# Performance work log

Hardware: AMD Instinct MI355X
Metric: run time of the kernel (lower is better)

Reference implementation:

```python
import jax, jax.numpy as jnp
import numpy as np

# Model dims
D = 64          # node channels (dim)
M = 16          # msg_channels
DEPTH = 3
VOCAB = 21      # num_atom_tokens
N = 100000      # nodes
E = 1600000     # directed edges
EIN = 2 * D + 1            # edge_mlp input: [x_i, x_j, |rel|^2]
EH = 2 * EIN               # dim_expansion * edge_input_dim
CH = 4 * M                 # 2 * dim_expansion * msg_channels
NH = 2 * D                 # dim_expansion * in_channels
INIT_STD = 1e-3            # init_eps normal init for Linear weights


def setup_inputs() -> dict:
    key = jax.random.key(0)
    ks = jax.random.split(key, 16)
    feats = jax.random.randint(ks[0], (N,), 0, VOCAB, dtype=jnp.int32)
    coors = jax.random.normal(ks[1], (N, 3), dtype=jnp.float32) * 10.0
    edge_index = jax.random.randint(ks[2], (2, E), 0, N, dtype=jnp.int32)
    emb = jax.random.normal(ks[3], (VOCAB, D), dtype=jnp.float32) * 0.1
    f32 = jnp.float32
    return {
        "feats": feats, "coors": coors, "edge_index": edge_index, "emb": emb,
        # edge_mlp: Linear(EIN->EH), SiLU, Linear(EH->M), SiLU
        "We1": jax.random.normal(ks[4], (DEPTH, EIN, EH), f32) * INIT_STD,
        "be1": jnp.zeros((DEPTH, EH), f32),
        "We2": jax.random.normal(ks[5], (DEPTH, EH, M), f32) * INIT_STD,
        "be2": jnp.zeros((DEPTH, M), f32),
        # coord_mlp: Linear(M->CH), SiLU, Linear(CH->1)
        "Wc1": jax.random.normal(ks[6], (DEPTH, M, CH), f32) * INIT_STD,
        "bc1": jnp.zeros((DEPTH, CH), f32),
        "Wc2": jax.random.normal(ks[7], (DEPTH, CH, 1), f32) * INIT_STD,
        "bc2": jnp.zeros((DEPTH, 1), f32),
        # node_mlp: Linear(D+M->NH), SiLU, Linear(NH->D)
        "Wn1": jax.random.normal(ks[8], (DEPTH, D + M, NH), f32) * INIT_STD,
        "bn1": jnp.zeros((DEPTH, NH), f32),
        "Wn2": jax.random.normal(ks[9], (DEPTH, NH, D), f32) * INIT_STD,
        "bn2": jnp.zeros((DEPTH, D), f32),
    }


def reference(feats, coors, edge_index, emb,
              We1, be1, We2, be2, Wc1, bc1, Wc2, bc2, Wn1, bn1, Wn2, bn2):
    # node_encoder: embedding lookup
    x = emb[feats]                       # [N, D]
    pos = coors                          # [N, 3]
    src = edge_index[0]                  # x_j / pos_j (source, flow source->target)
    tgt = edge_index[1]                  # x_i / pos_i (target) = scatter index
    n = x.shape[0]
    for l in range(DEPTH):
        # message: per-edge gather + MLPs
        rel = pos[tgt] - pos[src]                              # [E, 3]
        d2 = jnp.sum(rel * rel, axis=1, keepdims=True)         # [E, 1]
        m_in = jnp.concatenate([x[tgt], x[src], d2], axis=1)   # [E, 2D+1]
        h = jax.nn.silu(m_in @ We1[l] + be1[l])                # [E, EH]
        msg = jax.nn.silu(h @ We2[l] + be2[l])                 # [E, M]
        cw = jax.nn.silu(msg @ Wc1[l] + bc1[l]) @ Wc2[l] + bc2[l]  # [E, 1]
        pos_msg = rel * cw                                     # [E, 3] (coors_norm is Identity)
        # aggregate: scatter-add to target nodes
        agg_msg = jax.ops.segment_sum(msg, tgt, num_segments=n)      # [N, M]
        agg_pos = jax.ops.segment_sum(pos_msg, tgt, num_segments=n)  # [N, 3]
        # node update: node_norm is Identity
        nh = jax.nn.silu(jnp.concatenate([x, agg_msg], axis=1) @ Wn1[l] + bn1[l])
        out_x = nh @ Wn2[l] + bn2[l]                           # [N, D]
        pos = pos + agg_pos                                    # out_pos += pos (no velocity)
        x = x + out_x                                          # residual=True
    return x, pos
```

## Files before the change

kernel.cpp:

```cpp
#include <hip/hip_runtime.h>
#include <hip/hip_bf16.h>
#include <stdint.h>

#define NDIM   64
#define MDIM   16
#define NLAYER 3
#define EIN    129
#define EHD    258
#define CHD    64
#define NHD    128
#define NIN    80
#define AB_STRIDE 512
#define PKT_STRIDE 32
#define FP8_SCALE 1024.0f
#define NVALS  19

#define WE1F_L (34*2*512)
#define WN1F_L (8*3*512)
#define WN2F_L (4*4*512)
#define WE2F_L (9*512)
#define WC1F_L (4*512)

typedef float vf2 __attribute__((ext_vector_type(2)));
typedef __bf16 bf16x8 __attribute__((ext_vector_type(8)));
typedef float  f32x4  __attribute__((ext_vector_type(4)));

#define MFMA16(a, b, c) __builtin_amdgcn_mfma_f32_16x16x32_bf16((a), (b), (c), 0, 0, 0)

__device__ __forceinline__ float rcp_f(float x) { return __builtin_amdgcn_rcpf(x); }
#if __has_builtin(__builtin_amdgcn_exp2f)
__device__ __forceinline__ float exp2_f(float x) { return __builtin_amdgcn_exp2f(x); }
#else
__device__ __forceinline__ float exp2_f(float x) { return __expf(x * 0.6931471805599453f); }
#endif
__device__ __forceinline__ float silu_f(float v) {
    return v * rcp_f(1.0f + __expf(-v));
}
#define CC_EXP (-1.4426950408889634f / 1024.0f)
__device__ __forceinline__ float hprime_f(float u) {
    return u * rcp_f(1.0f + exp2_f(CC_EXP * u));
}
__device__ __forceinline__ float bflo(uint32_t u) {
    union { uint32_t u; float f; } c; c.u = u << 16; return c.f;
}
__device__ __forceinline__ float bfhi(uint32_t u) {
    union { uint32_t u; float f; } c; c.u = u & 0xffff0000u; return c.f;
}
__device__ __forceinline__ uint32_t pk_fp8_4(float f0, float f1, float f2, float f3) {
    uint32_t r = (uint32_t)__builtin_amdgcn_cvt_pk_fp8_f32(f0, f1, 0, false);
    r = (uint32_t)__builtin_amdgcn_cvt_pk_fp8_f32(f2, f3, (int)r, true);
    return r;
}
__device__ __forceinline__ float clamp8(float v) {
    return fminf(448.0f, fmaxf(-448.0f, v * FP8_SCALE));
}

__global__ void prep_kernel(const float* __restrict__ We1, const float* __restrict__ Wn1,
                            const float* __restrict__ Wn2, const float* __restrict__ We2,
                            const float* __restrict__ Wc1,
                            __bf16* __restrict__ WE1F, __bf16* __restrict__ WN1F,
                            __bf16* __restrict__ WN2F, __bf16* __restrict__ WE2F,
                            __bf16* __restrict__ WC1F) {
    int idx = blockIdx.x * 256 + threadIdx.x;
    const int T1 = NLAYER * WE1F_L;
    if (idx < T1) {
        int l  = idx / WE1F_L;
        int r  = idx % WE1F_L;
        int ct = r / 1024;
        int r2 = r % 1024;
        int kh = r2 / 512;
        int r3 = r2 % 512;
        int lane = r3 >> 3, jj = r3 & 7;
        int half = ct / 17, ctl = ct % 17;
        int col = ctl * 16 + (lane & 15);
        int k = kh * 32 + (lane >> 4) * 8 + jj;
        float v = 0.f;
        if (col < EHD) v = We1[((size_t)l * EIN + (half ? 64 + k : k)) * EHD + col];
        WE1F[idx] = (__bf16)v;
        return;
    }
    idx -= T1;
    const int T2 = NLAYER * WN1F_L;
    if (idx < T2) {
        int l  = idx / WN1F_L;
        int r  = idx % WN1F_L;
        int ct = r / 1536;
        int r2 = r % 1536;
        int kt = r2 / 512;
        int r3 = r2 % 512;
        int lane = r3 >> 3, jj = r3 & 7;
        int col = ct * 16 + (lane & 15);
        int k = kt * 32 + (lane >> 4) * 8 + jj;
        float v = (k < NIN) ? Wn1[((size_t)l * NIN + k) * NHD + col] : 0.f;
        WN1F[idx] = (__bf16)v;
        return;
    }
    idx -= T2;
    const int T3 = NLAYER * WN2F_L;
    if (idx < T3) {
        int l  = idx / WN2F_L;
        int r  = idx % WN2F_L;
        int ct = r / 2048;
        int r2 = r % 2048;
        int kt = r2 / 512;
        int r3 = r2 % 512;
        int lane = r3 >> 3, jj = r3 & 7;
        int col = ct * 16 + (lane & 15);
        int k = kt * 32 + (lane >> 4) * 8 + jj;
        WN2F[idx] = (__bf16)Wn2[((size_t)l * NHD + k) * NDIM + col];
        return;
    }
    idx -= T3;
    const int T4 = NLAYER * WE2F_L;
    if (idx < T4) {
        int l  = idx / WE2F_L;
        int r  = idx % WE2F_L;
        int kt = r / 512;
        int r3 = r % 512;
        int lane = r3 >> 3, jj = r3 & 7;
        int m = lane & 15;
        int k = kt * 32 + (lane >> 4) * 8 + jj;
        float v = (k < EHD) ? We2[((size_t)l * EHD + k) * MDIM + m] * (1.0f / FP8_SCALE) : 0.f;
        WE2F[idx] = (__bf16)v;
        return;
    }
    idx -= T4;
    const int T5 = NLAYER * WC1F_L;
    if (idx < T5) {
        int l  = idx / WC1F_L;
        int r  = idx % WC1F_L;
        int ct = r / 512;
        int r3 = r % 512;
        int lane = r3 >> 3, jj = r3 & 7;
        int c = ct * 16 + (lane & 15);
        int k = (lane >> 4) * 8 + jj;
        float v = (k < MDIM) ? Wc1[((size_t)l * MDIM + k) * CHD + c] : 0.f;
        WC1F[idx] = (__bf16)v;
    }
}

__global__ void init_kernel(const int* __restrict__ feats, const float* __restrict__ coors,
                            const float* __restrict__ emb,
                            float* __restrict__ x, float* __restrict__ pos, int N) {
    int idx = blockIdx.x * 256 + threadIdx.x;
    int nx = N * NDIM;
    if (idx < nx) {
        int n = idx >> 6, c = idx & 63;
        x[idx] = emb[feats[n] * NDIM + c];
    } else {
        int j = idx - nx;
        if (j < N * 3) pos[j] = coors[j];
    }
}

__global__ void hist_kernel(const int* __restrict__ ei, int* __restrict__ cnt, int E) {
    int e = blockIdx.x * 256 + threadIdx.x;
    if (e < E) atomicAdd(&cnt[ei[E + e]], 1);
}

__global__ void scan_sum_kernel(const int* __restrict__ cnt, int* __restrict__ bsum, int N) {
    __shared__ int ws[4];
    int i = blockIdx.x * 256 + threadIdx.x;
    int v = (i < N) ? cnt[i] : 0;
    #pragma unroll
    for (int off = 32; off; off >>= 1) v += __shfl_down(v, off);
    int lane = threadIdx.x & 63, w = threadIdx.x >> 6;
    if (lane == 0) ws[w] = v;
    __syncthreads();
    if (threadIdx.x == 0) bsum[blockIdx.x] = ws[0] + ws[1] + ws[2] + ws[3];
}
__global__ void __launch_bounds__(1024) scan_top_kernel(int* __restrict__ bsum, int nb) {
    __shared__ int ws[16];
    int tid = threadIdx.x, lane = tid & 63, w = tid >> 6;
    int v = (tid < nb) ? bsum[tid] : 0;
    int sc = v;
    #pragma unroll
    for (int off = 1; off < 64; off <<= 1) {
        int u = __shfl_up(sc, off);
        if (lane >= off) sc += u;
    }
    if (lane == 63) ws[w] = sc;
    __syncthreads();
    int woff = 0;
    #pragma unroll
    for (int k = 0; k < 16; ++k) woff += (k < w) ? ws[k] : 0;
    if (tid < nb) bsum[tid] = woff + sc - v;
}
__global__ void scan_fin_kernel(const int* __restrict__ cnt, const int* __restrict__ bsum,
                                int* __restrict__ cursor, int N) {
    __shared__ int ws[4];
    int i = blockIdx.x * 256 + threadIdx.x;
    int tid = threadIdx.x, lane = tid & 63, w = tid >> 6;
    int v = (i < N) ? cnt[i] : 0;
    int sc = v;
    #pragma unroll
    for (int off = 1; off < 64; off <<= 1) {
        int u = __shfl_up(sc, off);
        if (lane >= off) sc += u;
    }
    if (lane == 63) ws[w] = sc;
    __syncthreads();
    int woff = 0;
    #pragma unroll
    for (int k = 0; k < 4; ++k) woff += (k < w) ? ws[k] : 0;
    if (i < N) cursor[i] = bsum[blockIdx.x] + woff + sc - v;
}

__global__ void scatter_kernel(const int* __restrict__ ei, int* __restrict__ cursor,
                               uint2* __restrict__ sorted_st, int E) {
    int e = blockIdx.x * 256 + threadIdx.x;
    if (e >= E) return;
    int s = ei[e], t = ei[E + e];
    int p = atomicAdd(&cursor[t], 1);
    uint2 st; st.x = (uint32_t)s; st.y = (uint32_t)t;
    sorted_st[p] = st;
}

__global__ void __launch_bounds__(256) gemm_ab_mfma(
        const float* __restrict__ x, const float* __restrict__ pos,
        const bf16x8* __restrict__ WE1Fl, const float* __restrict__ be1l,
        uint8_t* __restrict__ A8, uint8_t* __restrict__ pkt,
        float* __restrict__ agg_msg, float* __restrict__ agg_pos, int N) {
    __shared__ __align__(16) __bf16 stg[4][16][280];
    int wave = threadIdx.x >> 6, lane = threadIdx.x & 63;
    int half = wave & 1;
    int nb = blockIdx.x * 32 + (wave >> 1) * 16;
    int lrow = lane & 15, lkg = lane >> 4;
    int row = nb + lrow; if (row >= N) row = N - 1;

    const float* xr = x + (size_t)row * NDIM + lkg * 8;
    bf16x8 a0, a1;
    #pragma unroll
    for (int j = 0; j < 8; ++j) { a0[j] = (__bf16)xr[j]; a1[j] = (__bf16)xr[32 + j]; }

    f32x4 acc[17];
    #pragma unroll
    for (int t = 0; t < 17; ++t) acc[t] = (f32x4){0.f, 0.f, 0.f, 0.f};
    const bf16x8* bf = WE1Fl + (size_t)(half * 17) * 2 * 64 + lane;
    #pragma unroll
    for (int t = 0; t < 17; ++t) {
        bf16x8 b0 = bf[(t * 2 + 0) * 64];
        bf16x8 b1 = bf[(t * 2 + 1) * 64];
        acc[t] = MFMA16(a0, b0, acc[t]);
        acc[t] = MFMA16(a1, b1, acc[t]);
    }
    #pragma unroll
    for (int t = 0; t < 17; ++t) {
        int col = t * 16 + lrow;
        float bias = (half == 0 && col < EHD) ? be1l[col] : 0.f;
        #pragma unroll
        for (int r = 0; r < 4; ++r)
            stg[wave][lkg * 4 + r][col] = (__bf16)(acc[t][r] + bias);
    }
    __syncthreads();

    int node = lane >> 2;
    int gnode = nb + node;
    const __bf16* hrow = &stg[wave][node][(lane & 3) * 64];
    if (gnode < N) {
        uint8_t* dst = A8 + (size_t)gnode * AB_STRIDE + half * 256 + (lane & 3) * 64;
        #pragma unroll
        for (int g = 0; g < 8; ++g) {
            bf16x8 hv = *(const bf16x8*)(hrow + g * 8);
            uint2 pk;
            pk.x = pk_fp8_4(clamp8((float)hv[0]), clamp8((float)hv[1]),
                            clamp8((float)hv[2]), clamp8((float)hv[3]));
            pk.y = pk_fp8_4(clamp8((float)hv[4]), clamp8((float)hv[5]),
                            clamp8((float)hv[6]), clamp8((float)hv[7]));
            *(uint2*)(dst + g * 8) = pk;
        }
    }
    if (lane < 16 && nb + lane < N) {
        int gn = nb + lane;
        const uint16_t* hr = (const uint16_t*)&stg[wave][lane][256];
        uint32_t ex = (uint32_t)hr[0] | ((uint32_t)hr[1] << 16);
        uint32_t* pk = (uint32_t*)(pkt + (size_t)gn * PKT_STRIDE);
        if (half == 0) {
            uint4 w0;
            w0.x = __float_as_uint(pos[3 * gn]);
            w0.y = __float_as_uint(pos[3 * gn + 1]);
            w0.z = __float_as_uint(pos[3 * gn + 2]);
            w0.w = ex;
            *(uint4*)pk = w0;
        } else {
            pk[4] = ex;
        }
    }
    {
        int i16 = blockIdx.x * 512 + (int)threadIdx.x * 2;
        if (i16 + 1 < N * MDIM) {
            *(vf2*)(agg_msg + i16) = (vf2){0.f, 0.f};
        } else if (i16 < N * MDIM) {
            agg_msg[i16] = 0.f;
        }
        if (threadIdx.x < 96) {
            int ip = blockIdx.x * 96 + (int)threadIdx.x;
            if (ip < N * 3) agg_pos[ip] = 0.f;
        }
    }
}

__global__ void __launch_bounds__(256) edge_kernel(
        const uint2* __restrict__ sorted_st,
        const uint8_t* __restrict__ A8, const uint8_t* __restrict__ pkt,
        const bf16x8* __restrict__ WE2Fl, const bf16x8* __restrict__ WC1Fl,
        const float* __restrict__ be2l,
        const float* __restrict__ bc1, const float* __restrict__ Wc2,
        const float* __restrict__ bc2, const float* __restrict__ w128,
        float* __restrict__ agg_msg, float* __restrict__ agg_pos, int E) {

    __shared__ __align__(16) vf2    w128p[132];
    __shared__ __align__(16) __bf16 msg_lds[4][64][24];
    __shared__ int  run_t[4][64];
    __shared__ uint run_se[4][64];

    int tid  = threadIdx.x;
    int wave = tid >> 6, lane = tid & 63;
    int kg   = lane >> 4, lrow = lane & 15;

    int base = blockIdx.x * 256 + wave * 64;
    int eo = base + lane;
    bool active = (eo < E);
    int eoc = active ? eo : (E - 1);
    uint2 st = sorted_st[eoc];
    int s_own = (int)st.x;
    int t_ld  = (int)st.y;
    int t_scan = active ? t_ld : -1;

    const uint32_t* ppt = (const uint32_t*)(pkt + (size_t)t_ld  * PKT_STRIDE);
    const uint32_t* pps = (const uint32_t*)(pkt + (size_t)s_own * PKT_STRIDE);
    uint4 pt0 = *(const uint4*)ppt;
    uint4 ps0 = *(const uint4*)pps;
    uint32_t b2o = pps[4];
    uint32_t a2o = pt0.w;
    float rx = __uint_as_float(pt0.x) - __uint_as_float(ps0.x);
    float ry = __uint_as_float(pt0.y) - __uint_as_float(ps0.y);
    float rz = __uint_as_float(pt0.z) - __uint_as_float(ps0.z);
    float d2o = rx*rx + ry*ry + rz*rz;

    bf16x8 bw[9];
    #pragma unroll
    for (int kt = 0; kt < 9; ++kt) bw[kt] = WE2Fl[kt * 64 + lane];
    bf16x8 bwc[4];
    float bc1r[4], wc2r[4];
    #pragma unroll
    for (int ct = 0; ct < 4; ++ct) {
        bwc[ct]  = WC1Fl[ct * 64 + lane];
        bc1r[ct] = bc1[ct * 16 + lrow];
        wc2r[ct] = Wc2[ct * 16 + lrow];
    }
    float be2m = be2l[lrow];
    float cb2  = bc2[0];

    for (int i = tid; i < 132; i += 256) {
        int k0 = i * 2;
        float lo = (k0     < EHD) ? w128[k0]     * FP8_SCALE : 0.f;
        float hi = (k0 + 1 < EHD) ? w128[k0 + 1] * FP8_SCALE : 0.f;
        w128p[i] = (vf2){lo, hi};
    }
    __syncthreads();

    #pragma unroll
    for (int tt = 0; tt < 4; ++tt) {
        int srcl = tt * 16 + lrow;
        int t_r = __shfl(t_ld, srcl);
        int s_r = __shfl(s_own, srcl);
        float d2r = __shfl(d2o, srcl);
        uint32_t a2r = (uint32_t)__shfl((int)a2o, srcl);
        uint32_t b2r = (uint32_t)__shfl((int)b2o, srcl);
        vf2 d2v = (vf2){d2r, d2r};

        const uint8_t* Ar = A8 + (size_t)t_r * AB_STRIDE + kg * 8;
        const uint8_t* Br = A8 + (size_t)s_r * AB_STRIDE + 256 + kg * 8;

        f32x4 acc = (f32x4){0.f, 0.f, 0.f, 0.f};
        #pragma unroll
        for (int kt = 0; kt < 8; ++kt) {
            uint2 ad = *(const uint2*)(Ar + kt * 32);
            uint2 bd = *(const uint2*)(Br + kt * 32);
            const vf2* wp = &w128p[kt * 16 + kg * 4];
            vf2 u0 = __builtin_amdgcn_cvt_pk_f32_fp8(ad.x, false)
                   + __builtin_amdgcn_cvt_pk_f32_fp8(bd.x, false) + d2v * wp[0];
            vf2 u1 = __builtin_amdgcn_cvt_pk_f32_fp8(ad.x, true)
                   + __builtin_amdgcn_cvt_pk_f32_fp8(bd.x, true)  + d2v * wp[1];
            vf2 u2 = __builtin_amdgcn_cvt_pk_f32_fp8(ad.y, false)
                   + __builtin_amdgcn_cvt_pk_f32_fp8(bd.y, false) + d2v * wp[2];
            vf2 u3 = __builtin_amdgcn_cvt_pk_f32_fp8(ad.y, true)
                   + __builtin_amdgcn_cvt_pk_f32_fp8(bd.y, true)  + d2v * wp[3];
            bf16x8 af;
            af[0] = (__bf16)hprime_f(u0.x); af[1] = (__bf16)hprime_f(u0.y);
            af[2] = (__bf16)hprime_f(u1.x); af[3] = (__bf16)hprime_f(u1.y);
            af[4] = (__bf16)hprime_f(u2.x); af[5] = (__bf16)hprime_f(u2.y);
            af[6] = (__bf16)hprime_f(u3.x); af[7] = (__bf16)hprime_f(u3.y);
            acc = MFMA16(af, bw[kt], acc);
        }
        {
            float h0 = 0.f, h1 = 0.f;
            if (kg == 0) {
                vf2 wx = w128p[128];
                float u0 = (bflo(a2r) + bflo(b2r)) * FP8_SCALE + d2r * wx.x;
                float u1 = (bfhi(a2r) + bfhi(b2r)) * FP8_SCALE + d2r * wx.y;
                h0 = hprime_f(u0);
                h1 = hprime_f(u1);
            }
            bf16x8 af;
            af[0] = (__bf16)h0; af[1] = (__bf16)h1;
            #pragma unroll
            for (int j = 2; j < 8; ++j) af[j] = (__bf16)0.f;
            acc = MFMA16(af, bw[8], acc);
        }
        #pragma unroll
        for (int r = 0; r < 4; ++r) {
            float mval = silu_f(acc[r] + be2m);
            msg_lds[wave][tt * 16 + kg * 4 + r][lrow] = (__bf16)mval;
        }
        __builtin_amdgcn_wave_barrier();

        bf16x8 ac = (bf16x8){(__bf16)0.f,(__bf16)0.f,(__bf16)0.f,(__bf16)0.f,
                             (__bf16)0.f,(__bf16)0.f,(__bf16)0.f,(__bf16)0.f};
        if (kg < 2) ac = *(const bf16x8*)&msg_lds[wave][tt * 16 + lrow][kg * 8];
        f32x4 c0 = (f32x4){0.f,0.f,0.f,0.f}, c1 = c0, c2 = c0, c3 = c0;
        c0 = MFMA16(ac, bwc[0], c0);
        c1 = MFMA16(ac, bwc[1], c1);
        c2 = MFMA16(ac, bwc[2], c2);
        c3 = MFMA16(ac, bwc[3], c3);
        float p0 = 0.f, p1 = 0.f, p2 = 0.f, p3 = 0.f;
        p0 += silu_f(c0[0] + bc1r[0]) * wc2r[0]; p1 += silu_f(c0[1] + bc1r[0]) * wc2r[0];
        p2 += silu_f(c0[2] + bc1r[0]) * wc2r[0]; p3 += silu_f(c0[3] + bc1r[0]) * wc2r[0];
        p0 += silu_f(c1[0] + bc1r[1]) * wc2r[1]; p1 += silu_f(c1[1] + bc1r[1]) * wc2r[1];
        p2 += silu_f(c1[2] + bc1r[1]) * wc2r[1]; p3 += silu_f(c1[3] + bc1r[1]) * wc2r[1];
        p0 += silu_f(c2[0] + bc1r[2]) * wc2r[2]; p1 += silu_f(c2[1] + bc1r[2]) * wc2r[2];
        p2 += silu_f(c2[2] + bc1r[2]) * wc2r[2]; p3 += silu_f(c2[3] + bc1r[2]) * wc2r[2];
        p0 += silu_f(c3[0] + bc1r[3]) * wc2r[3]; p1 += silu_f(c3[1] + bc1r[3]) * wc2r[3];
        p2 += silu_f(c3[2] + bc1r[3]) * wc2r[3]; p3 += silu_f(c3[3] + bc1r[3]) * wc2r[3];
        #pragma unroll
        for (int mk = 1; mk < 16; mk <<= 1) {
            p0 += __shfl_xor(p0, mk);
            p1 += __shfl_xor(p1, mk);
            p2 += __shfl_xor(p2, mk);
            p3 += __shfl_xor(p3, mk);
        }
        if (lrow < 4) {
            float sel = (lrow == 0) ? p0 : (lrow == 1) ? p1 : (lrow == 2) ? p2 : p3;
            msg_lds[wave][tt * 16 + kg * 4 + lrow][16] = (__bf16)(cb2 + sel);
        }
        __builtin_amdgcn_wave_barrier();
    }

    float cwo = (float)msg_lds[wave][lane][16];
    msg_lds[wave][lane][16] = (__bf16)(rx * cwo);
    msg_lds[wave][lane][17] = (__bf16)(ry * cwo);
    msg_lds[wave][lane][18] = (__bf16)(rz * cwo);

    int t_next = __shfl_down(t_scan, 1);
    bool is_end = (lane == 63) || (t_next != t_scan);
    uint64_t mask = __ballot(is_end);
    int nr = __popcll(mask);
    if (is_end) {
        uint64_t below = mask & ((1ULL << lane) - 1ULL);
        int rid = __popcll(below);
        int st2 = (below == 0ULL) ? 0 : (64 - __builtin_clzll(below));
        run_t[wave][rid]  = t_scan;
        run_se[wave][rid] = (uint)((st2 << 8) | lane);
    }
    __builtin_amdgcn_wave_barrier();

    for (int task = lane; task < nr * NVALS; task += 64) {
        int rid = task / NVALS;
        int v   = task - rid * NVALS;
        int t   = run_t[wave][rid];
        if (t >= 0) {
            uint se = run_se[wave][rid];
            int st2 = (int)(se >> 8), en = (int)(se & 0xFFu);
            float sum = 0.f;
            for (int e = st2; e <= en; ++e) sum += (float)msg_lds[wave][e][v];
            if (v < 16) atomicAdd(&agg_msg[(size_t)t * MDIM + v], sum);
            else        atomicAdd(&agg_pos[(size_t)t * 3 + (v - 16)], sum);
        }
    }
}

__global__ void __launch_bounds__(256) node_mfma(
        float* __restrict__ x, float* __restrict__ pos,
        const float* __restrict__ agg_msg, const float* __restrict__ agg_pos,
        const bf16x8* __restrict__ WN1Fl, const bf16x8* __restrict__ WN2Fl,
        const float* __restrict__ bn1l, const float* __restrict__ bn2l, int N) {
    __shared__ __align__(16) __bf16 stg[4][16][136];
    int wave = threadIdx.x >> 6, lane = threadIdx.x & 63;
    int nb = blockIdx.x * 64 + wave * 16;
    int lrow = lane & 15, lkg = lane >> 4;
    int row = nb + lrow;
    int rc = (row < N) ? row : (N - 1);

    const float* xr = x + (size_t)rc * NDIM + lkg * 8;
    bf16x8 a0, a1, a2;
    #pragma unroll
    for (int j = 0; j < 8; ++j) { a0[j] = (__bf16)xr[j]; a1[j] = (__bf16)xr[32 + j]; }
    if (lkg < 2) {
        const float* mr = agg_msg + (size_t)rc * MDIM + lkg * 8;
        #pragma unroll
        for (int j = 0; j < 8; ++j) a2[j] = (__bf16)mr[j];
    } else {
        #pragma unroll
        for (int j = 0; j < 8; ++j) a2[j] = (__bf16)0.f;
    }

    f32x4 h[8];
    #pragma unroll
    for (int t = 0; t < 8; ++t) h[t] = (f32x4){0.f, 0.f, 0.f, 0.f};
    const bf16x8* b1 = WN1Fl + lane;
    #pragma unroll
    for (int t = 0; t < 8; ++t) {
        h[t] = MFMA16(a0, b1[(t * 3 + 0) * 64], h[t]);
        h[t] = MFMA16(a1, b1[(t * 3 + 1) * 64], h[t]);
        h[t] = MFMA16(a2, b1[(t * 3 + 2) * 64], h[t]);
    }
    #pragma unroll
    for (int t = 0; t < 8; ++t) {
        int col = t * 16 + lrow;
        float bias = bn1l[col];
        #pragma unroll
        for (int r = 0; r < 4; ++r)
            stg[wave][lkg * 4 + r][col] = (__bf16)silu_f(h[t][r] + bias);
    }
    __syncthreads();

    bf16x8 af[4];
    #pragma unroll
    for (int kt = 0; kt < 4; ++kt)
        af[kt] = *(const bf16x8*)&stg[wave][lrow][kt * 32 + lkg * 8];

    f32x4 o[4];
    #pragma unroll
    for (int t = 0; t < 4; ++t) o[t] = (f32x4){0.f, 0.f, 0.f, 0.f};
    const bf16x8* b2 = WN2Fl + lane;
    #pragma unroll
    for (int t = 0; t < 4; ++t) {
        #pragma unroll
        for (int kt = 0; kt < 4; ++kt)
            o[t] = MFMA16(af[kt], b2[(t * 4 + kt) * 64], o[t]);
    }

    int orow = nb + lkg * 4;
    #pragma unroll
    for (int t = 0; t < 4; ++t) {
        int col = t * 16 + lrow;
        float bias = bn2l[col];
        #pragma unroll
        for (int r = 0; r < 4; ++r) {
            int rr = orow + r;
            if (rr < N) x[(size_t)rr * NDIM + col] += o[t][r] + bias;
        }
    }
    if (threadIdx.x < 192) {
        long j = (long)blockIdx.x * 192 + threadIdx.x;
        if (j < (long)N * 3) pos[j] += agg_pos[j];
    }
}

extern "C" void kernel_launch(void* const* d_in, const int* in_sizes, int n_in,
                              void* d_out, int out_size, void* d_ws, size_t ws_size,
                              hipStream_t stream) {
    const int*   feats = (const int*)  d_in[0];
    const float* coors = (const float*)d_in[1];
    const int*   ei    = (const int*)  d_in[2];
    const float* emb   = (const float*)d_in[3];
    const float* We1   = (const float*)d_in[4];
    const float* be1   = (const float*)d_in[5];
    const float* We2   = (const float*)d_in[6];
    const float* be2   = (const float*)d_in[7];
    const float* Wc1   = (const float*)d_in[8];
    const float* bc1   = (const float*)d_in[9];
    const float* Wc2   = (const float*)d_in[10];
    const float* bc2   = (const float*)d_in[11];
    const float* Wn1   = (const float*)d_in[12];
    const float* bn1   = (const float*)d_in[13];
    const float* Wn2   = (const float*)d_in[14];
    const float* bn2   = (const float*)d_in[15];

    const int N = in_sizes[0];
    const int E = in_sizes[2] / 2;

    float* x   = (float*)d_out;
    float* pos = (float*)d_out + (size_t)N * NDIM;

    char* w = (char*)d_ws;
    uint8_t* A8 = (uint8_t*)w;
    size_t off = ((size_t)N * AB_STRIDE + 255) & ~(size_t)255;
    uint8_t* pkt = (uint8_t*)(w + off);
    off += ((size_t)N * PKT_STRIDE + 255) & ~(size_t)255;
    float* agg_msg = (float*)(w + off);
    off += ((size_t)N * MDIM * 4 + 255) & ~(size_t)255;
    float* agg_pos = (float*)(w + off);
    off += ((size_t)N * 3 * 4 + 255) & ~(size_t)255;
    uint2* sorted_st = (uint2*)(w + off);
    off += ((size_t)E * 8 + 255) & ~(size_t)255;
    int* cnt = (int*)(w + off);
    off += ((size_t)N * 4 + 255) & ~(size_t)255;
    int* cursor = (int*)(w + off);
    off += ((size_t)N * 4 + 255) & ~(size_t)255;
    int* bsum = (int*)(w + off);
    off += (((size_t)N / 256 + 2) * 4 + 255) & ~(size_t)255;
    __bf16* WE1F = (__bf16*)(w + off);
    off += ((size_t)NLAYER * WE1F_L * 2 + 255) & ~(size_t)255;
    __bf16* WN1F = (__bf16*)(w + off);
    off += ((size_t)NLAYER * WN1F_L * 2 + 255) & ~(size_t)255;
    __bf16* WN2F = (__bf16*)(w + off);
    off += ((size_t)NLAYER * WN2F_L * 2 + 255) & ~(size_t)255;
    __bf16* WE2F = (__bf16*)(w + off);
    off += ((size_t)NLAYER * WE2F_L * 2 + 255) & ~(size_t)255;
    __bf16* WC1F = (__bf16*)(w + off);
    (void)ws_size; (void)n_in; (void)out_size;

    {
        int total = NLAYER * (WE1F_L + WN1F_L + WN2F_L + WE2F_L + WC1F_L);
        prep_kernel<<<(total + 255) / 256, 256, 0, stream>>>(We1, Wn1, Wn2, We2, Wc1,
                                                             WE1F, WN1F, WN2F, WE2F, WC1F);
    }
    {
        int total = N * (NDIM + 3);
        init_kernel<<<(total + 255) / 256, 256, 0, stream>>>(feats, coors, emb, x, pos, N);
    }
    hipMemsetAsync(cnt, 0, (size_t)N * 4, stream);
    hist_kernel<<<(E + 255) / 256, 256, 0, stream>>>(ei, cnt, E);
    {
        int nb = (N + 255) / 256;
        scan_sum_kernel<<<nb, 256, 0, stream>>>(cnt, bsum, N);
        scan_top_kernel<<<1, 1024, 0, stream>>>(bsum, nb);
        scan_fin_kernel<<<nb, 256, 0, stream>>>(cnt, bsum, cursor, N);
    }
    scatter_kernel<<<(E + 255) / 256, 256, 0, stream>>>(ei, cursor, sorted_st, E);

    for (int l = 0; l < NLAYER; ++l) {
        const float* We1_l  = We1 + (size_t)l * EIN * EHD;
        const float* w128_l = We1_l + (size_t)128 * EHD;

        gemm_ab_mfma<<<(N + 31) / 32, 256, 0, stream>>>(
            x, pos, (const bf16x8*)(WE1F + (size_t)l * WE1F_L),
            be1 + (size_t)l * EHD, A8, pkt, agg_msg, agg_pos, N);

        edge_kernel<<<(E + 255) / 256, 256, 0, stream>>>(
            sorted_st, A8, pkt,
            (const bf16x8*)(WE2F + (size_t)l * WE2F_L),
            (const bf16x8*)(WC1F + (size_t)l * WC1F_L),
            be2 + (size_t)l * MDIM,
            bc1 + (size_t)l * CHD, Wc2 + (size_t)l * CHD, bc2 + l, w128_l,
            agg_msg, agg_pos, E);

        node_mfma<<<(N + 63) / 64, 256, 0, stream>>>(
            x, pos, agg_msg, agg_pos,
            (const bf16x8*)(WN1F + (size_t)l * WN1F_L),
            (const bf16x8*)(WN2F + (size_t)l * WN2F_L),
            bn1 + (size_t)l * NHD, bn2 + (size_t)l * NDIM, N);
    }
}
```

Measured before the change: 1.047 ms.

## Precompute layer-0 node projections per vocab token and batch sigmoid reciprocals

In layer 0, x is just an embedding lookup, so the per-node A/B projection is computed once per vocabulary token (21 rows) and then gathered to all nodes by a new copy kernel. This replaces the full N-row GEMM for that layer. Separately, the edge kernel's SiLU and h' activations are computed four at a time with a shared reciprocal (sig4), cutting reciprocal instructions at the cost of extra multiplies and a clamp against overflow. The gemm_ab kernel run on vocab rows still reads pos and zeroes agg buffers for only VOCAB rows, so gather_ab handles the zeroing and the pos packet.

Measured after the change: 1.068 ms. No clear change (+2.0%).

```diff
diff --git a/kernel.cpp b/kernel.cpp
--- a/kernel.cpp
+++ b/kernel.cpp
@@ -37,8 +37,24 @@
     return v * rcp_f(1.0f + __expf(-v));
 }
 #define CC_EXP (-1.4426950408889634f / 1024.0f)
+#define CC_SILU (-1.4426950408889634f)
 __device__ __forceinline__ float hprime_f(float u) {
     return u * rcp_f(1.0f + exp2_f(CC_EXP * u));
+}
+__device__ __forceinline__ void sig4(vf2 x01, vf2 x23, float c, float* s) {
+    vf2 cv = (vf2){c, c};
+    vf2 a01 = x01 * cv, a23 = x23 * cv;
+    a01.x = fminf(a01.x, 25.f); a01.y = fminf(a01.y, 25.f);
+    a23.x = fminf(a23.x, 25.f); a23.y = fminf(a23.y, 25.f);
+    float d0 = 1.f + exp2_f(a01.x), d1 = 1.f + exp2_f(a01.y);
+    float d2 = 1.f + exp2_f(a23.x), d3 = 1.f + exp2_f(a23.y);
+    float p01 = d0 * d1, p23 = d2 * d3;
+    float r = rcp_f(p01 * p23);
+    float r01 = r * p23, r23 = r * p01;
+    s[0] = x01.x * (r01 * d1);
+    s[1] = x01.y * (r01 * d0);
+    s[2] = x23.x * (r23 * d3);
+    s[3] = x23.y * (r23 * d2);
 }
 __device__ __forceinline__ float bflo(uint32_t u) {
     union { uint32_t u; float f; } c; c.u = u << 16; return c.f;
@@ -300,6 +316,44 @@
     }
 }
 
+__global__ void __launch_bounds__(256) gather_ab(
+        const int* __restrict__ feats, const float* __restrict__ pos,
+        const uint8_t* __restrict__ A8v, const uint8_t* __restrict__ pktv,
+        uint8_t* __restrict__ A8, uint8_t* __restrict__ pkt,
+        float* __restrict__ agg_msg, float* __restrict__ agg_pos, int N) {
+    int nb = blockIdx.x * 8;
+    int t = threadIdx.x;
+    int node = nb + (t >> 5);
+    int chunk = t & 31;
+    if (node < N) {
+        int tok = feats[node];
+        const uint4* src = (const uint4*)(A8v + (size_t)tok * AB_STRIDE);
+        uint4* dst = (uint4*)(A8 + (size_t)node * AB_STRIDE);
+        dst[chunk] = src[chunk];
+    }
+    if (t < 128) {
+        int i = nb * MDIM + t;
+        if (i < N * MDIM) agg_msg[i] = 0.f;
+    } else if (t < 152) {
+        int i = nb * 3 + (t - 128);
+        if (i < N * 3) agg_pos[i] = 0.f;
+    } else if (t < 160) {
+        int n = nb + (t - 152);
+        if (n < N) {
+            int tok = feats[n];
+            const uint32_t* pv = (const uint32_t*)(pktv + (size_t)tok * PKT_STRIDE);
+            uint32_t* pk = (uint32_t*)(pkt + (size_t)n * PKT_STRIDE);
+            uint4 w0;
+            w0.x = __float_as_uint(pos[3 * n]);
+            w0.y = __float_as_uint(pos[3 * n + 1]);
+            w0.z = __float_as_uint(pos[3 * n + 2]);
+            w0.w = pv[3];
+            *(uint4*)pk = w0;
+            pk[4] = pv[4];
+        }
+    }
+}
+
 __global__ void __launch_bounds__(256) edge_kernel(
         const uint2* __restrict__ sorted_st,
         const uint8_t* __restrict__ A8, const uint8_t* __restrict__ pkt,
@@ -387,11 +441,14 @@
                    + __builtin_amdgcn_cvt_pk_f32_fp8(bd.y, false) + d2v * wp[2];
             vf2 u3 = __builtin_amdgcn_cvt_pk_f32_fp8(ad.y, true)
                    + __builtin_amdgcn_cvt_pk_f32_fp8(bd.y, true)  + d2v * wp[3];
+            float ha[4], hb[4];
+            sig4(u0, u1, CC_EXP, ha);
+            sig4(u2, u3, CC_EXP, hb);
             bf16x8 af;
-            af[0] = (__bf16)hprime_f(u0.x); af[1] = (__bf16)hprime_f(u0.y);
-            af[2] = (__bf16)hprime_f(u1.x); af[3] = (__bf16)hprime_f(u1.y);
-            af[4] = (__bf16)hprime_f(u2.x); af[5] = (__bf16)hprime_f(u2.y);
-            af[6] = (__bf16)hprime_f(u3.x); af[7] = (__bf16)hprime_f(u3.y);
+            af[0] = (__bf16)ha[0]; af[1] = (__bf16)ha[1];
+            af[2] = (__bf16)ha[2]; af[3] = (__bf16)ha[3];
+            af[4] = (__bf16)hb[0]; af[5] = (__bf16)hb[1];
+            af[6] = (__bf16)hb[2]; af[7] = (__bf16)hb[3];
             acc = MFMA16(af, bw[kt], acc);
         }
         {
@@ -409,10 +466,14 @@
             for (int j = 2; j < 8; ++j) af[j] = (__bf16)0.f;
             acc = MFMA16(af, bw[8], acc);
         }
-        #pragma unroll
-        for (int r = 0; r < 4; ++r) {
-            float mval = silu_f(acc[r] + be2m);
-            msg_lds[wave][tt * 16 + kg * 4 + r][lrow] = (__bf16)mval;
+        {
+            vf2 m01 = (vf2){acc[0] + be2m, acc[1] + be2m};
+            vf2 m23 = (vf2){acc[2] + be2m, acc[3] + be2m};
+            float ms[4];
+            sig4(m01, m23, CC_SILU, ms);
+            #pragma unroll
+            for (int r = 0; r < 4; ++r)
+                msg_lds[wave][tt * 16 + kg * 4 + r][lrow] = (__bf16)ms[r];
         }
         __builtin_amdgcn_wave_barrier();
 
@@ -424,15 +485,16 @@
         c1 = MFMA16(ac, bwc[1], c1);
         c2 = MFMA16(ac, bwc[2], c2);
         c3 = MFMA16(ac, bwc[3], c3);
-        float p0 = 0.f, p1 = 0.f, p2 = 0.f, p3 = 0.f;
-        p0 += silu_f(c0[0] + bc1r[0]) * wc2r[0]; p1 += silu_f(c0[1] + bc1r[0]) * wc2r[0];
-        p2 += silu_f(c0[2] + bc1r[0]) * wc2r[0]; p3 += silu_f(c0[3] + bc1r[0]) * wc2r[0];
-        p0 += silu_f(c1[0] + bc1r[1]) * wc2r[1]; p1 += silu_f(c1[1] + bc1r[1]) * wc2r[1];
-        p2 += silu_f(c1[2] + bc1r[1]) * wc2r[1]; p3 += silu_f(c1[3] + bc1r[1]) * wc2r[1];
-        p0 += silu_f(c2[0] + bc1r[2]) * wc2r[2]; p1 += silu_f(c2[1] + bc1r[2]) * wc2r[2];
-        p2 += silu_f(c2[2] + bc1r[2]) * wc2r[2]; p3 += silu_f(c2[3] + bc1r[2]) * wc2r[2];
-        p0 += silu_f(c3[0] + bc1r[3]) * wc2r[3]; p1 += silu_f(c3[1] + bc1r[3]) * wc2r[3];
-        p2 += silu_f(c3[2] + bc1r[3]) * wc2r[3]; p3 += silu_f(c3[3] + bc1r[3]) * wc2r[3];
+        float pr[4];
+        #pragma unroll
+        for (int r = 0; r < 4; ++r) {
+            vf2 v01 = (vf2){c0[r] + bc1r[0], c1[r] + bc1r[1]};
+            vf2 v23 = (vf2){c2[r] + bc1r[2], c3[r] + bc1r[3]};
+            float s[4];
+            sig4(v01, v23, CC_SILU, s);
+            pr[r] = s[0]*wc2r[0] + s[1]*wc2r[1] + s[2]*wc2r[2] + s[3]*wc2r[3];
+        }
+        float p0 = pr[0], p1 = pr[1], p2 = pr[2], p3 = pr[3];
         #pragma unroll
         for (int mk = 1; mk < 16; mk <<= 1) {
             p0 += __shfl_xor(p0, mk);
@@ -580,6 +642,7 @@
 
     const int N = in_sizes[0];
     const int E = in_sizes[2] / 2;
+    const int VOCAB = in_sizes[3] / NDIM;
 
     float* x   = (float*)d_out;
     float* pos = (float*)d_out + (size_t)N * NDIM;
@@ -601,6 +664,10 @@
     off += ((size_t)N * 4 + 255) & ~(size_t)255;
     int* bsum = (int*)(w + off);
     off += (((size_t)N / 256 + 2) * 4 + 255) & ~(size_t)255;
+    uint8_t* A8v = (uint8_t*)(w + off);
+    off += (size_t)32 * AB_STRIDE;
+    uint8_t* pktv = (uint8_t*)(w + off);
+    off += (size_t)32 * PKT_STRIDE;
     __bf16* WE1F = (__bf16*)(w + off);
     off += ((size_t)NLAYER * WE1F_L * 2 + 255) & ~(size_t)255;
     __bf16* WN1F = (__bf16*)(w + off);
@@ -635,9 +702,17 @@
         const float* We1_l  = We1 + (size_t)l * EIN * EHD;
         const float* w128_l = We1_l + (size_t)128 * EHD;
 
-        gemm_ab_mfma<<<(N + 31) / 32, 256, 0, stream>>>(
-            x, pos, (const bf16x8*)(WE1F + (size_t)l * WE1F_L),
-            be1 + (size_t)l * EHD, A8, pkt, agg_msg, agg_pos, N);
+        if (l == 0) {
+            gemm_ab_mfma<<<(VOCAB + 31) / 32, 256, 0, stream>>>(
+                emb, pos, (const bf16x8*)(WE1F + (size_t)l * WE1F_L),
+                be1 + (size_t)l * EHD, A8v, pktv, agg_msg, agg_pos, VOCAB);
+            gather_ab<<<(N + 7) / 8, 256, 0, stream>>>(
+                feats, pos, A8v, pktv, A8, pkt, agg_msg, agg_pos, N);
+        } else {
+            gemm_ab_mfma<<<(N + 31) / 32, 256, 0, stream>>>(
+                x, pos, (const bf16x8*)(WE1F + (size_t)l * WE1F_L),
+                be1 + (size_t)l * EHD, A8, pkt, agg_msg, agg_pos, N);
+        }
 
         edge_kernel<<<(E + 255) / 256, 256, 0, stream>>>(
             sorted_st, A8, pkt,
```
